# Kernel optimization log

Hardware: AMD Instinct MI355X
Metric: run time of the kernel (lower is better)

## Reference

```python
import jax, jax.numpy as jnp
import numpy as np

N = 30000      # nodes
E = 480000     # edges (avg degree 16)
IN = 128       # input_size
HID = 128      # hidden_size
H = 4          # heads
C = HID // H   # channels per head = 32
NEG_SLOPE = 0.2


def gat_layer(x, src, dst, W, al, ar, act):
    """DGL-style GATConv: x (N, Fin) -> (N, h*c). al, ar: (h, c)."""
    n = x.shape[0]
    h, c = al.shape
    f = (x @ W).reshape(n, h, c)                      # projected features
    el = jnp.sum(f * al, axis=-1)                     # (N, h)
    er = jnp.sum(f * ar, axis=-1)                     # (N, h)
    e = jax.nn.leaky_relu(el[src] + er[dst], NEG_SLOPE)  # (E, h) edge scores
    # edge softmax over incoming edges of each dst node
    m = jax.lax.stop_gradient(jax.ops.segment_max(e, dst, num_segments=n))
    a = jnp.exp(e - m[dst])
    z = jax.ops.segment_sum(a, dst, num_segments=n)   # (N, h)
    alpha = a / z[dst]                                # (E, h)
    out = jax.ops.segment_sum(alpha[:, :, None] * f[src], dst, num_segments=n)
    out = out.reshape(n, h * c)
    return act(out) if act is not None else out


def setup_inputs() -> dict:
    key = jax.random.key(0)
    ks = jax.random.split(key, 14)
    s = 0.1
    return {
        "inputs": jax.random.normal(ks[0], (N, IN), jnp.float32),
        "src": jax.random.randint(ks[1], (E,), 0, N, dtype=jnp.int32),
        "dst": jax.random.randint(ks[2], (E,), 0, N, dtype=jnp.int32),
        "W0": jax.random.normal(ks[3], (IN, H * C), jnp.float32) * s,
        "al0": jax.random.normal(ks[4], (H, C), jnp.float32) * s,
        "ar0": jax.random.normal(ks[5], (H, C), jnp.float32) * s,
        "W1": jax.random.normal(ks[6], (H * C, H * C), jnp.float32) * s,
        "al1": jax.random.normal(ks[7], (H, C), jnp.float32) * s,
        "ar1": jax.random.normal(ks[8], (H, C), jnp.float32) * s,
        "W2": jax.random.normal(ks[9], (H * C, H * HID), jnp.float32) * s,
        "al2": jax.random.normal(ks[10], (H, HID), jnp.float32) * s,
        "ar2": jax.random.normal(ks[11], (H, HID), jnp.float32) * s,
        "fc_w": jax.random.normal(ks[12], (H * HID, 8), jnp.float32) * s,
        "fc_b": jnp.zeros((8,), jnp.float32),
    }


def reference(inputs, src, dst, W0, al0, ar0, W1, al1, ar1, W2, al2, ar2, fc_w, fc_b):
    h = gat_layer(inputs, src, dst, W0, al0, ar0, jax.nn.relu)
    h = gat_layer(h, src, dst, W1, al1, ar1, jax.nn.relu)
    h = gat_layer(h, src, dst, W2, al2, ar2, None)      # (N, H*HID)
    h = jax.nn.relu(h)                                  # dropout p=0 is identity
    pooled = jnp.max(h, axis=0, keepdims=True)          # global max pooling -> (1, H*HID)
    logits = pooled @ fc_w + fc_b                       # (1, 8)
    return jax.nn.softmax(logits, axis=-1)
```

## Files before the change

### kernel.cpp

```cpp
#include <hip/hip_runtime.h>

#define HH 4

typedef __attribute__((ext_vector_type(8))) short bf16x8;
typedef __attribute__((ext_vector_type(4))) float f32x4;

__device__ __forceinline__ float lrelu(float v) { return (v >= 0.0f) ? v : 0.2f * v; }

__device__ __forceinline__ unsigned short f2bf(float x) {
    union { float f; unsigned u; } v; v.f = x;
    unsigned r = (v.u + 0x7FFFu + ((v.u >> 16) & 1u)) >> 16;
    return (unsigned short)r;
}
__device__ __forceinline__ float bf2f(unsigned short b) {
    union { unsigned u; float f; } v; v.u = ((unsigned)b) << 16;
    return v.f;
}

__global__ void zero_kernel(int* __restrict__ p, int n) {
    int i = blockIdx.x * blockDim.x + threadIdx.x;
    if (i < n) p[i] = 0;
}

__global__ void hist_kernel(const int* __restrict__ dst, int* __restrict__ deg, int E) {
    int i = blockIdx.x * blockDim.x + threadIdx.x;
    if (i < E) atomicAdd(&deg[dst[i]], 1);
}

__global__ void scan_block(const int* __restrict__ deg, int* __restrict__ rs,
                           int* __restrict__ bsum, int n) {
    __shared__ int buf[1024];
    int i = blockIdx.x * 1024 + threadIdx.x;
    int v = (i < n) ? deg[i] : 0;
    buf[threadIdx.x] = v;
    __syncthreads();
    for (int off = 1; off < 1024; off <<= 1) {
        int t = (threadIdx.x >= off) ? buf[threadIdx.x - off] : 0;
        __syncthreads();
        buf[threadIdx.x] += t;
        __syncthreads();
    }
    if (i < n) rs[i + 1] = buf[threadIdx.x];
    if (threadIdx.x == 1023) bsum[blockIdx.x] = buf[1023];
}

__global__ void scan_top(int* bsum, int nb) {
    if (threadIdx.x == 0 && blockIdx.x == 0) {
        int acc = 0;
        for (int b = 0; b < nb; ++b) { int t = bsum[b]; bsum[b] = acc; acc += t; }
    }
}

__global__ void scan_add(int* __restrict__ rs, const int* __restrict__ bsum, int n) {
    int i = blockIdx.x * blockDim.x + threadIdx.x;
    if (i == 0) rs[0] = 0;
    if (i < n) rs[i + 1] += bsum[i >> 10];
}

__global__ void scatter_kernel(const int* __restrict__ src, const int* __restrict__ dst,
                               const int* __restrict__ rs, int* __restrict__ cur,
                               int* __restrict__ csrc, int E) {
    int i = blockIdx.x * blockDim.x + threadIdx.x;
    if (i >= E) return;
    int d = dst[i];
    int p = rs[d] + atomicAdd(&cur[d], 1);
    csrc[p] = src[i];
}

__global__ void prep_all(const float* __restrict__ W0, const float* __restrict__ W1,
                         const float* __restrict__ W2, const float* __restrict__ al2,
                         const float* __restrict__ ar2, bf16x8* __restrict__ WFH,
                         bf16x8* __restrict__ WFL, float* __restrict__ wl,
                         float* __restrict__ wr) {
    if (blockIdx.x < 48) {
        const int wid = blockIdx.x * 4 + (threadIdx.x >> 6);
        const int l = threadIdx.x & 63;
        const int lr = l & 15, lg = l >> 4;
        int t = wid;
        const float* srcp;
        int stride, coff;
        if (t < 32) { srcp = W0; stride = 128; coff = 0; }
        else if (t < 64) { srcp = W1; stride = 128; coff = 0; t -= 32; }
        else { t -= 64; srcp = W2; stride = 512; coff = (t >> 5) * 128; t &= 31; }
        const int kt = t >> 3, ct = t & 7;
        bf16x8 h8, l8;
#pragma unroll
        for (int j = 0; j < 8; ++j) {
            float w = srcp[(size_t)(kt * 32 + lg * 8 + j) * stride + coff + ct * 16 + lr];
            unsigned short hb = f2bf(w);
            h8[j] = (short)hb;
            l8[j] = (short)f2bf(w - bf2f(hb));
        }
        WFH[(size_t)wid * 64 + l] = h8;
        WFL[(size_t)wid * 64 + l] = l8;
    } else {
        int idx = threadIdx.x;
#pragma unroll
        for (int k = 0; k < 2; ++k, idx += 256) {
            int h = idx >> 7, i = idx & 127;
            float sl = 0.0f, sr = 0.0f;
            for (int c = 0; c < 128; ++c) {
                float w = W2[(size_t)i * 512 + h * 128 + c];
                sl = fmaf(w, al2[h * 128 + c], sl);
                sr = fmaf(w, ar2[h * 128 + c], sr);
            }
            wl[idx] = sl;
            wr[idx] = sr;
        }
    }
}

__global__ __launch_bounds__(256) void mfma_gemm128(const float* __restrict__ x,
                                                    const bf16x8* __restrict__ BH,
                                                    const bf16x8* __restrict__ BL,
                                                    unsigned short* __restrict__ fbf,
                                                    const float* __restrict__ al,
                                                    const float* __restrict__ ar,
                                                    float* __restrict__ el,
                                                    float* __restrict__ er, int n) {
    const int tid = threadIdx.x;
    const int w = tid >> 6, l = tid & 63;
    const int lr = l & 15, lg = l >> 4;
    const int rowbase = blockIdx.x * 64 + w * 16;
    const int arow = rowbase + lr;

    f32x4 acc[8];
#pragma unroll
    for (int ct = 0; ct < 8; ++ct) acc[ct] = (f32x4){0.f, 0.f, 0.f, 0.f};

    for (int kt = 0; kt < 4; ++kt) {
        float a[8];
        if (arow < n) {
            float4 p0 = *reinterpret_cast<const float4*>(&x[(size_t)arow * 128 + kt * 32 + lg * 8]);
            float4 p1 = *reinterpret_cast<const float4*>(&x[(size_t)arow * 128 + kt * 32 + lg * 8 + 4]);
            a[0] = p0.x; a[1] = p0.y; a[2] = p0.z; a[3] = p0.w;
            a[4] = p1.x; a[5] = p1.y; a[6] = p1.z; a[7] = p1.w;
        } else {
#pragma unroll
            for (int j = 0; j < 8; ++j) a[j] = 0.f;
        }
        bf16x8 ah, alo;
#pragma unroll
        for (int j = 0; j < 8; ++j) {
            unsigned short hb = f2bf(a[j]);
            ah[j] = (short)hb;
            alo[j] = (short)f2bf(a[j] - bf2f(hb));
        }
        const bf16x8* bh = &BH[(size_t)(kt * 8) * 64 + l];
        const bf16x8* bl = &BL[(size_t)(kt * 8) * 64 + l];
#pragma unroll
        for (int ct = 0; ct < 8; ++ct) {
            bf16x8 b1 = bh[ct * 64];
            bf16x8 b2 = bl[ct * 64];
            acc[ct] = __builtin_amdgcn_mfma_f32_16x16x32_bf16(ah, b1, acc[ct], 0, 0, 0);
            acc[ct] = __builtin_amdgcn_mfma_f32_16x16x32_bf16(alo, b1, acc[ct], 0, 0, 0);
            acc[ct] = __builtin_amdgcn_mfma_f32_16x16x32_bf16(ah, b2, acc[ct], 0, 0, 0);
        }
    }
#pragma unroll
    for (int reg = 0; reg < 4; ++reg) {
        int orow = rowbase + lg * 4 + reg;
        if (orow < n) {
#pragma unroll
            for (int ct = 0; ct < 8; ++ct)
                fbf[(size_t)orow * 128 + ct * 16 + lr] = f2bf(acc[ct][reg]);
        }
    }
    float pel[4][4], per_[4][4];
#pragma unroll
    for (int h = 0; h < 4; ++h) {
        float a0 = al[h * 32 + lr], a1 = al[h * 32 + 16 + lr];
        float r0 = ar[h * 32 + lr], r1 = ar[h * 32 + 16 + lr];
#pragma unroll
        for (int reg = 0; reg < 4; ++reg) {
            pel[reg][h] = acc[2 * h][reg] * a0 + acc[2 * h + 1][reg] * a1;
            per_[reg][h] = acc[2 * h][reg] * r0 + acc[2 * h + 1][reg] * r1;
        }
    }
#pragma unroll
    for (int off = 1; off < 16; off <<= 1) {
#pragma unroll
        for (int reg = 0; reg < 4; ++reg)
#pragma unroll
            for (int h = 0; h < 4; ++h) {
                pel[reg][h] += __shfl_xor(pel[reg][h], off);
                per_[reg][h] += __shfl_xor(per_[reg][h], off);
            }
    }
    if (lr == 0) {
#pragma unroll
        for (int reg = 0; reg < 4; ++reg) {
            int orow = rowbase + lg * 4 + reg;
            if (orow < n) {
#pragma unroll
                for (int h = 0; h < 4; ++h) {
                    el[orow * HH + h] = pel[reg][h];
                    er[orow * HH + h] = per_[reg][h];
                }
            }
        }
    }
}

__global__ __launch_bounds__(256) void mfma_bd_pool(const unsigned short* __restrict__ aggbf,
                                                    const bf16x8* __restrict__ WFH,
                                                    const bf16x8* __restrict__ WFL,
                                                    unsigned* __restrict__ pooled, int n) {
    __shared__ float smax[4][128];
    const int tid = threadIdx.x;
    const int w = tid >> 6, l = tid & 63;
    const int lr = l & 15, lg = l >> 4;
    const int y = blockIdx.y;
    const int rowbase = blockIdx.x * 64 + w * 16;
    const int arow = rowbase + lr;
    const bf16x8* BH = WFH + (size_t)(64 + y * 32) * 64;
    const bf16x8* BL = WFL + (size_t)(64 + y * 32) * 64;

    f32x4 acc[8];
#pragma unroll
    for (int ct = 0; ct < 8; ++ct) acc[ct] = (f32x4){0.f, 0.f, 0.f, 0.f};

    for (int kt = 0; kt < 4; ++kt) {
        bf16x8 av = {0, 0, 0, 0, 0, 0, 0, 0};
        if (arow < n)
            av = *reinterpret_cast<const bf16x8*>(&aggbf[(size_t)arow * 512 + y * 128 + kt * 32 + lg * 8]);
        const bf16x8* bh = &BH[(size_t)(kt * 8) * 64 + l];
        const bf16x8* bl = &BL[(size_t)(kt * 8) * 64 + l];
#pragma unroll
        for (int ct = 0; ct < 8; ++ct) {
            acc[ct] = __builtin_amdgcn_mfma_f32_16x16x32_bf16(av, bh[ct * 64], acc[ct], 0, 0, 0);
            acc[ct] = __builtin_amdgcn_mfma_f32_16x16x32_bf16(av, bl[ct * 64], acc[ct], 0, 0, 0);
        }
    }
    float cm[8];
#pragma unroll
    for (int ct = 0; ct < 8; ++ct) {
        float v = fmaxf(fmaxf(acc[ct][0], acc[ct][1]), fmaxf(acc[ct][2], acc[ct][3]));
        cm[ct] = fmaxf(v, 0.f);
    }
#pragma unroll
    for (int ct = 0; ct < 8; ++ct) {
        cm[ct] = fmaxf(cm[ct], __shfl_xor(cm[ct], 16));
        cm[ct] = fmaxf(cm[ct], __shfl_xor(cm[ct], 32));
    }
    if (l < 16) {
#pragma unroll
        for (int ct = 0; ct < 8; ++ct) smax[w][ct * 16 + lr] = cm[ct];
    }
    __syncthreads();
    if (tid < 128) {
        float mx = fmaxf(fmaxf(smax[0][tid], smax[1][tid]), fmaxf(smax[2][tid], smax[3][tid]));
        atomicMax(&pooled[y * 128 + tid], __float_as_uint(mx));
    }
}

template <int MODE>
__global__ __launch_bounds__(256) void aggr_wave128(const int* __restrict__ rs,
                                                    const int* __restrict__ csrc,
                                                    const float* __restrict__ el,
                                                    const float* __restrict__ er,
                                                    const unsigned short* __restrict__ fbf,
                                                    float* __restrict__ out,
                                                    unsigned short* __restrict__ outbf,
                                                    const float* __restrict__ wl,
                                                    const float* __restrict__ wr,
                                                    float* __restrict__ el2,
                                                    float* __restrict__ er2, int n) {
    const int d = blockIdx.x * 4 + (threadIdx.x >> 6);
    if (d >= n) return;
    const int lane = threadIdx.x & 63;
    const int hg = lane >> 4, j16 = lane & 15;
    const int hw = lane >> 5;
    const int L31 = lane & 31;
    const int cb4 = L31 * 4;
    const int myh = L31 >> 3;
    const int e0 = rs[d], e1 = rs[d + 1];
    const float erd = er[d * HH + hg];

    float4 acc = {0.f, 0.f, 0.f, 0.f};
    float zacc = 0.f;
    for (int c0 = e0; c0 < e1; c0 += 16) {
        const int cnt = min(16, e1 - c0);
        int s_mine = 0;
        float wmine = 0.f;
        if (j16 < cnt) {
            s_mine = csrc[c0 + j16];
            wmine = __expf(lrelu(el[s_mine * HH + hg] + erd));
        }
        zacc += wmine;
        const int pairs = cnt >> 1;
#pragma unroll 4
        for (int jj = 0; jj < pairs; ++jj) {
            int idx = 2 * jj + hw;
            int s = __shfl(s_mine, idx);
            float wv = __shfl(wmine, myh * 16 + idx);
            ushort4 xu = *reinterpret_cast<const ushort4*>(&fbf[(size_t)s * 128 + cb4]);
            acc.x = fmaf(wv, bf2f(xu.x), acc.x);
            acc.y = fmaf(wv, bf2f(xu.y), acc.y);
            acc.z = fmaf(wv, bf2f(xu.z), acc.z);
            acc.w = fmaf(wv, bf2f(xu.w), acc.w);
        }
        if (cnt & 1) {
            int idx = cnt - 1;
            int s = __shfl(s_mine, idx);
            float wv = __shfl(wmine, myh * 16 + idx);
            if (hw) wv = 0.f;
            ushort4 xu = *reinterpret_cast<const ushort4*>(&fbf[(size_t)s * 128 + cb4]);
            acc.x = fmaf(wv, bf2f(xu.x), acc.x);
            acc.y = fmaf(wv, bf2f(xu.y), acc.y);
            acc.z = fmaf(wv, bf2f(xu.z), acc.z);
            acc.w = fmaf(wv, bf2f(xu.w), acc.w);
        }
    }
    float zh = zacc;
#pragma unroll
    for (int off = 1; off < 16; off <<= 1) zh += __shfl_xor(zh, off);
    float zmy = __shfl(zh, myh * 16);
    const float rz = (zmy > 0.f) ? 1.0f / zmy : 0.f;
    acc.x += __shfl_xor(acc.x, 32);
    acc.y += __shfl_xor(acc.y, 32);
    acc.z += __shfl_xor(acc.z, 32);
    acc.w += __shfl_xor(acc.w, 32);
    acc.x = fmaxf(acc.x * rz, 0.f);
    acc.y = fmaxf(acc.y * rz, 0.f);
    acc.z = fmaxf(acc.z * rz, 0.f);
    acc.w = fmaxf(acc.w * rz, 0.f);
    if (MODE == 0) {
        if (hw == 0) *reinterpret_cast<float4*>(&out[(size_t)d * 128 + cb4]) = acc;
    } else {
        if (hw == 0) {
            ushort4 sv;
            sv.x = f2bf(acc.x); sv.y = f2bf(acc.y); sv.z = f2bf(acc.z); sv.w = f2bf(acc.w);
            *reinterpret_cast<ushort4*>(&outbf[(size_t)d * 128 + cb4]) = sv;
        }
        float pl[4], pr[4];
#pragma unroll
        for (int h = 0; h < 4; ++h) {
            float4 wlv = *reinterpret_cast<const float4*>(&wl[h * 128 + cb4]);
            float4 wrv = *reinterpret_cast<const float4*>(&wr[h * 128 + cb4]);
            pl[h] = acc.x * wlv.x + acc.y * wlv.y + acc.z * wlv.z + acc.w * wlv.w;
            pr[h] = acc.x * wrv.x + acc.y * wrv.y + acc.z * wrv.z + acc.w * wrv.w;
        }
#pragma unroll
        for (int off = 1; off < 32; off <<= 1) {
#pragma unroll
            for (int h = 0; h < 4; ++h) {
                pl[h] += __shfl_xor(pl[h], off);
                pr[h] += __shfl_xor(pr[h], off);
            }
        }
        if (lane == 0) {
#pragma unroll
            for (int h = 0; h < 4; ++h) {
                el2[d * HH + h] = pl[h];
                er2[d * HH + h] = pr[h];
            }
        }
    }
}

__global__ __launch_bounds__(256) void aggr_x(const int* __restrict__ rs,
                                              const int* __restrict__ csrc,
                                              const float* __restrict__ el,
                                              const float* __restrict__ er,
                                              const unsigned short* __restrict__ xbf,
                                              unsigned short* __restrict__ aggbf, int n) {
    const int d = blockIdx.x * 4 + (threadIdx.x >> 6);
    if (d >= n) return;
    const int lane = threadIdx.x & 63;
    const int hg = lane >> 4, j16 = lane & 15;
    const int hw = lane >> 5;
    const int L31 = lane & 31;
    const int cb4 = L31 * 4;
    const int e0 = rs[d], e1 = rs[d + 1];
    const float erd = er[d * HH + hg];

    float4 acc[4];
#pragma unroll
    for (int h = 0; h < 4; ++h) acc[h] = (float4){0.f, 0.f, 0.f, 0.f};
    float zacc = 0.f;
    for (int c0 = e0; c0 < e1; c0 += 16) {
        const int cnt = min(16, e1 - c0);
        int s_mine = 0;
        float wmine = 0.f;
        if (j16 < cnt) {
            s_mine = csrc[c0 + j16];
            wmine = __expf(lrelu(el[s_mine * HH + hg] + erd));
        }
        zacc += wmine;
        const int pairs = cnt >> 1;
#pragma unroll 2
        for (int jj = 0; jj < pairs; ++jj) {
            int idx = 2 * jj + hw;
            int s = __shfl(s_mine, idx);
            float w0 = __shfl(wmine, idx);
            float w1 = __shfl(wmine, 16 + idx);
            float w2 = __shfl(wmine, 32 + idx);
            float w3 = __shfl(wmine, 48 + idx);
            ushort4 xu = *reinterpret_cast<const ushort4*>(&xbf[(size_t)s * 128 + cb4]);
            float x0 = bf2f(xu.x), x1 = bf2f(xu.y), x2 = bf2f(xu.z), x3 = bf2f(xu.w);
            acc[0].x = fmaf(w0, x0, acc[0].x); acc[0].y = fmaf(w0, x1, acc[0].y);
            acc[0].z = fmaf(w0, x2, acc[0].z); acc[0].w = fmaf(w0, x3, acc[0].w);
            acc[1].x = fmaf(w1, x0, acc[1].x); acc[1].y = fmaf(w1, x1, acc[1].y);
            acc[1].z = fmaf(w1, x2, acc[1].z); acc[1].w = fmaf(w1, x3, acc[1].w);
            acc[2].x = fmaf(w2, x0, acc[2].x); acc[2].y = fmaf(w2, x1, acc[2].y);
            acc[2].z = fmaf(w2, x2, acc[2].z); acc[2].w = fmaf(w2, x3, acc[2].w);
            acc[3].x = fmaf(w3, x0, acc[3].x); acc[3].y = fmaf(w3, x1, acc[3].y);
            acc[3].z = fmaf(w3, x2, acc[3].z); acc[3].w = fmaf(w3, x3, acc[3].w);
        }
        if (cnt & 1) {
            int idx = cnt - 1;
            int s = __shfl(s_mine, idx);
            float m = hw ? 0.f : 1.f;
            float w0 = m * __shfl(wmine, idx);
            float w1 = m * __shfl(wmine, 16 + idx);
            float w2 = m * __shfl(wmine, 32 + idx);
            float w3 = m * __shfl(wmine, 48 + idx);
            ushort4 xu = *reinterpret_cast<const ushort4*>(&xbf[(size_t)s * 128 + cb4]);
            float x0 = bf2f(xu.x), x1 = bf2f(xu.y), x2 = bf2f(xu.z), x3 = bf2f(xu.w);
            acc[0].x = fmaf(w0, x0, acc[0].x); acc[0].y = fmaf(w0, x1, acc[0].y);
            acc[0].z = fmaf(w0, x2, acc[0].z); acc[0].w = fmaf(w0, x3, acc[0].w);
            acc[1].x = fmaf(w1, x0, acc[1].x); acc[1].y = fmaf(w1, x1, acc[1].y);
            acc[1].z = fmaf(w1, x2, acc[1].z); acc[1].w = fmaf(w1, x3, acc[1].w);
            acc[2].x = fmaf(w2, x0, acc[2].x); acc[2].y = fmaf(w2, x1, acc[2].y);
            acc[2].z = fmaf(w2, x2, acc[2].z); acc[2].w = fmaf(w2, x3, acc[2].w);
            acc[3].x = fmaf(w3, x0, acc[3].x); acc[3].y = fmaf(w3, x1, acc[3].y);
            acc[3].z = fmaf(w3, x2, acc[3].z); acc[3].w = fmaf(w3, x3, acc[3].w);
        }
    }
    float zh = zacc;
#pragma unroll
    for (int off = 1; off < 16; off <<= 1) zh += __shfl_xor(zh, off);
    float rzh[4];
#pragma unroll
    for (int h = 0; h < 4; ++h) {
        float zv = __shfl(zh, h * 16);
        rzh[h] = (zv > 0.f) ? 1.0f / zv : 0.f;
    }
#pragma unroll
    for (int h = 0; h < 4; ++h) {
        acc[h].x += __shfl_xor(acc[h].x, 32);
        acc[h].y += __shfl_xor(acc[h].y, 32);
        acc[h].z += __shfl_xor(acc[h].z, 32);
        acc[h].w += __shfl_xor(acc[h].w, 32);
        acc[h].x *= rzh[h]; acc[h].y *= rzh[h]; acc[h].z *= rzh[h]; acc[h].w *= rzh[h];
    }
    if (hw == 0) {
#pragma unroll
        for (int h = 0; h < 4; ++h) {
            ushort4 sv;
            sv.x = f2bf(acc[h].x); sv.y = f2bf(acc[h].y);
            sv.z = f2bf(acc[h].z); sv.w = f2bf(acc[h].w);
            *reinterpret_cast<ushort4*>(&aggbf[(size_t)d * 512 + h * 128 + cb4]) = sv;
        }
    }
}

__global__ void head_kernel(const float* __restrict__ pooled, const float* __restrict__ fcw,
                            const float* __restrict__ fcb, float* __restrict__ out) {
    __shared__ float logits[8];
    int t = threadIdx.x;
    if (t < 8) {
        float acc = fcb[t];
        for (int i = 0; i < 512; ++i) acc = fmaf(pooled[i], fcw[i * 8 + t], acc);
        logits[t] = acc;
    }
    __syncthreads();
    if (t == 0) {
        float mx = -1e30f;
        for (int j = 0; j < 8; ++j) mx = fmaxf(mx, logits[j]);
        float ex[8], s = 0.0f;
        for (int j = 0; j < 8; ++j) { ex[j] = expf(logits[j] - mx); s += ex[j]; }
        for (int j = 0; j < 8; ++j) out[j] = ex[j] / s;
    }
}

extern "C" void kernel_launch(void* const* d_in, const int* in_sizes, int n_in,
                              void* d_out, int out_size, void* d_ws, size_t ws_size,
                              hipStream_t stream) {
    const float* x0  = (const float*)d_in[0];
    const int*   src = (const int*)d_in[1];
    const int*   dst = (const int*)d_in[2];
    const float* W0  = (const float*)d_in[3];
    const float* al0 = (const float*)d_in[4];
    const float* ar0 = (const float*)d_in[5];
    const float* W1  = (const float*)d_in[6];
    const float* al1 = (const float*)d_in[7];
    const float* ar1 = (const float*)d_in[8];
    const float* W2  = (const float*)d_in[9];
    const float* al2 = (const float*)d_in[10];
    const float* ar2 = (const float*)d_in[11];
    const float* fcw = (const float*)d_in[12];
    const float* fcb = (const float*)d_in[13];
    float* outp = (float*)d_out;

    const int N = in_sizes[0] / 128;
    const int E = in_sizes[1];

    float* B0   = (float*)d_ws;
    float* el   = B0 + (size_t)N * 128;
    float* er   = el + (size_t)N * HH;
    float* el2  = er + (size_t)N * HH;
    float* er2  = el2 + (size_t)N * HH;
    float* wl   = er2 + (size_t)N * HH;
    float* wr   = wl + 512;
    int* deg  = (int*)(wr + 512);
    int* cur  = deg + N;
    float* pooled = (float*)(cur + N);
    int* rs   = (int*)(pooled + 512);
    int* bsum = rs + (N + 1);
    int* csrc = bsum + 64;
    unsigned short* Fbf   = (unsigned short*)(csrc + E);
    unsigned short* B1bf  = Fbf + (size_t)N * 128;
    unsigned short* AGGbf = B1bf + (size_t)N * 128;
    uintptr_t wfaddr = ((uintptr_t)(AGGbf + (size_t)N * 512) + 15) & ~(uintptr_t)15;
    bf16x8* WFH = (bf16x8*)wfaddr;
    bf16x8* WFL = WFH + (size_t)192 * 64;

    const int nzero = 2 * N + 512;
    zero_kernel<<<(nzero + 255) / 256, 256, 0, stream>>>(deg, nzero);
    prep_all<<<49, 256, 0, stream>>>(W0, W1, W2, al2, ar2, WFH, WFL, wl, wr);
    hist_kernel<<<(E + 255) / 256, 256, 0, stream>>>(dst, deg, E);
    const int nb = (N + 1023) / 1024;
    scan_block<<<nb, 1024, 0, stream>>>(deg, rs, bsum, N);
    scan_top<<<1, 64, 0, stream>>>(bsum, nb);
    scan_add<<<(N + 255) / 256, 256, 0, stream>>>(rs, bsum, N);
    scatter_kernel<<<(E + 255) / 256, 256, 0, stream>>>(src, dst, rs, cur, csrc, E);

    const int rowTiles = (N + 63) / 64;
    const int nodeBlocks = (N + 3) / 4;

    mfma_gemm128<<<rowTiles, 256, 0, stream>>>(x0, WFH, WFL, Fbf, al0, ar0, el, er, N);
    aggr_wave128<0><<<nodeBlocks, 256, 0, stream>>>(rs, csrc, el, er, Fbf, B0, nullptr,
                                                    nullptr, nullptr, nullptr, nullptr, N);
    mfma_gemm128<<<rowTiles, 256, 0, stream>>>(B0, WFH + (size_t)32 * 64, WFL + (size_t)32 * 64,
                                               Fbf, al1, ar1, el, er, N);
    aggr_wave128<1><<<nodeBlocks, 256, 0, stream>>>(rs, csrc, el, er, Fbf, nullptr, B1bf,
                                                    wl, wr, el2, er2, N);
    aggr_x<<<nodeBlocks, 256, 0, stream>>>(rs, csrc, el2, er2, B1bf, AGGbf, N);
    mfma_bd_pool<<<dim3(rowTiles, 4), 256, 0, stream>>>(AGGbf, WFH, WFL, (unsigned*)pooled, N);

    head_kernel<<<1, 64, 0, stream>>>(pooled, fcw, fcb, outp);
}
```

Before: 263.7 us.

## Process one edge per iteration across full wavefront in GAT aggregation kernels

Both aggregation kernels drop the 16-edge chunked scheme with shuffles and half-wave splitting. Instead every lane walks all incoming edges itself and recomputes the edge weight, and the row range is made wave-uniform with readfirstlane. In aggr_wave128 each lane now owns 2 channels, so no cross-half reduction is needed. In aggr_x each lane handles 8 channels of one head. This removes shuffle and reduction overhead, but every lane now repeats the csrc/el loads and the exp per edge, and the edge-level parallelism that hid gather latency is lost.

```diff
diff --git a/kernel.cpp b/kernel.cpp
--- a/kernel.cpp
+++ b/kernel.cpp
@@ -14,6 +14,14 @@
 }
 __device__ __forceinline__ float bf2f(unsigned short b) {
     union { unsigned u; float f; } v; v.u = ((unsigned)b) << 16;
+    return v.f;
+}
+__device__ __forceinline__ float bf2f_lo(unsigned u) {
+    union { unsigned x; float f; } v; v.x = u << 16;
+    return v.f;
+}
+__device__ __forceinline__ float bf2f_hi(unsigned u) {
+    union { unsigned x; float f; } v; v.x = u & 0xffff0000u;
     return v.f;
 }
 
@@ -266,83 +274,46 @@
                                                     const float* __restrict__ wr,
                                                     float* __restrict__ el2,
                                                     float* __restrict__ er2, int n) {
-    const int d = blockIdx.x * 4 + (threadIdx.x >> 6);
+    int d = blockIdx.x * 4 + (threadIdx.x >> 6);
     if (d >= n) return;
+    d = __builtin_amdgcn_readfirstlane(d);
     const int lane = threadIdx.x & 63;
-    const int hg = lane >> 4, j16 = lane & 15;
-    const int hw = lane >> 5;
-    const int L31 = lane & 31;
-    const int cb4 = L31 * 4;
-    const int myh = L31 >> 3;
-    const int e0 = rs[d], e1 = rs[d + 1];
+    const int hg = lane >> 4;
+    const int cb2 = lane * 2;
+    const int e0 = __builtin_amdgcn_readfirstlane(rs[d]);
+    const int e1 = __builtin_amdgcn_readfirstlane(rs[d + 1]);
     const float erd = er[d * HH + hg];
 
-    float4 acc = {0.f, 0.f, 0.f, 0.f};
-    float zacc = 0.f;
-    for (int c0 = e0; c0 < e1; c0 += 16) {
-        const int cnt = min(16, e1 - c0);
-        int s_mine = 0;
-        float wmine = 0.f;
-        if (j16 < cnt) {
-            s_mine = csrc[c0 + j16];
-            wmine = __expf(lrelu(el[s_mine * HH + hg] + erd));
-        }
-        zacc += wmine;
-        const int pairs = cnt >> 1;
+    float z = 0.f, a0 = 0.f, a1 = 0.f;
 #pragma unroll 4
-        for (int jj = 0; jj < pairs; ++jj) {
-            int idx = 2 * jj + hw;
-            int s = __shfl(s_mine, idx);
-            float wv = __shfl(wmine, myh * 16 + idx);
-            ushort4 xu = *reinterpret_cast<const ushort4*>(&fbf[(size_t)s * 128 + cb4]);
-            acc.x = fmaf(wv, bf2f(xu.x), acc.x);
-            acc.y = fmaf(wv, bf2f(xu.y), acc.y);
-            acc.z = fmaf(wv, bf2f(xu.z), acc.z);
-            acc.w = fmaf(wv, bf2f(xu.w), acc.w);
-        }
-        if (cnt & 1) {
-            int idx = cnt - 1;
-            int s = __shfl(s_mine, idx);
-            float wv = __shfl(wmine, myh * 16 + idx);
-            if (hw) wv = 0.f;
-            ushort4 xu = *reinterpret_cast<const ushort4*>(&fbf[(size_t)s * 128 + cb4]);
-            acc.x = fmaf(wv, bf2f(xu.x), acc.x);
-            acc.y = fmaf(wv, bf2f(xu.y), acc.y);
-            acc.z = fmaf(wv, bf2f(xu.z), acc.z);
-            acc.w = fmaf(wv, bf2f(xu.w), acc.w);
-        }
-    }
-    float zh = zacc;
-#pragma unroll
-    for (int off = 1; off < 16; off <<= 1) zh += __shfl_xor(zh, off);
-    float zmy = __shfl(zh, myh * 16);
-    const float rz = (zmy > 0.f) ? 1.0f / zmy : 0.f;
-    acc.x += __shfl_xor(acc.x, 32);
-    acc.y += __shfl_xor(acc.y, 32);
-    acc.z += __shfl_xor(acc.z, 32);
-    acc.w += __shfl_xor(acc.w, 32);
-    acc.x = fmaxf(acc.x * rz, 0.f);
-    acc.y = fmaxf(acc.y * rz, 0.f);
-    acc.z = fmaxf(acc.z * rz, 0.f);
-    acc.w = fmaxf(acc.w * rz, 0.f);
+    for (int e = e0; e < e1; ++e) {
+        int s = csrc[e];
+        float v = el[s * HH + hg] + erd;
+        float wv = __expf(lrelu(v));
+        z += wv;
+        unsigned xu = *reinterpret_cast<const unsigned*>(&fbf[(size_t)s * 128 + cb2]);
+        a0 = fmaf(wv, bf2f_lo(xu), a0);
+        a1 = fmaf(wv, bf2f_hi(xu), a1);
+    }
+    const float rz = (z > 0.f) ? 1.0f / z : 0.f;
+    a0 = fmaxf(a0 * rz, 0.f);
+    a1 = fmaxf(a1 * rz, 0.f);
     if (MODE == 0) {
-        if (hw == 0) *reinterpret_cast<float4*>(&out[(size_t)d * 128 + cb4]) = acc;
+        *reinterpret_cast<float2*>(&out[(size_t)d * 128 + cb2]) = make_float2(a0, a1);
     } else {
-        if (hw == 0) {
-            ushort4 sv;
-            sv.x = f2bf(acc.x); sv.y = f2bf(acc.y); sv.z = f2bf(acc.z); sv.w = f2bf(acc.w);
-            *reinterpret_cast<ushort4*>(&outbf[(size_t)d * 128 + cb4]) = sv;
-        }
+        ushort2 sv;
+        sv.x = f2bf(a0); sv.y = f2bf(a1);
+        *reinterpret_cast<ushort2*>(&outbf[(size_t)d * 128 + cb2]) = sv;
         float pl[4], pr[4];
 #pragma unroll
         for (int h = 0; h < 4; ++h) {
-            float4 wlv = *reinterpret_cast<const float4*>(&wl[h * 128 + cb4]);
-            float4 wrv = *reinterpret_cast<const float4*>(&wr[h * 128 + cb4]);
-            pl[h] = acc.x * wlv.x + acc.y * wlv.y + acc.z * wlv.z + acc.w * wlv.w;
-            pr[h] = acc.x * wrv.x + acc.y * wrv.y + acc.z * wrv.z + acc.w * wrv.w;
-        }
-#pragma unroll
-        for (int off = 1; off < 32; off <<= 1) {
+            float2 wlv = *reinterpret_cast<const float2*>(&wl[h * 128 + cb2]);
+            float2 wrv = *reinterpret_cast<const float2*>(&wr[h * 128 + cb2]);
+            pl[h] = a0 * wlv.x + a1 * wlv.y;
+            pr[h] = a0 * wrv.x + a1 * wrv.y;
+        }
+#pragma unroll
+        for (int off = 1; off < 64; off <<= 1) {
 #pragma unroll
             for (int h = 0; h < 4; ++h) {
                 pl[h] += __shfl_xor(pl[h], off);
@@ -365,95 +336,44 @@
                                               const float* __restrict__ er,
                                               const unsigned short* __restrict__ xbf,
                                               unsigned short* __restrict__ aggbf, int n) {
-    const int d = blockIdx.x * 4 + (threadIdx.x >> 6);
+    int d = blockIdx.x * 4 + (threadIdx.x >> 6);
     if (d >= n) return;
+    d = __builtin_amdgcn_readfirstlane(d);
     const int lane = threadIdx.x & 63;
     const int hg = lane >> 4, j16 = lane & 15;
-    const int hw = lane >> 5;
-    const int L31 = lane & 31;
-    const int cb4 = L31 * 4;
-    const int e0 = rs[d], e1 = rs[d + 1];
+    const int e0 = __builtin_amdgcn_readfirstlane(rs[d]);
+    const int e1 = __builtin_amdgcn_readfirstlane(rs[d + 1]);
     const float erd = er[d * HH + hg];
 
-    float4 acc[4];
-#pragma unroll
-    for (int h = 0; h < 4; ++h) acc[h] = (float4){0.f, 0.f, 0.f, 0.f};
-    float zacc = 0.f;
-    for (int c0 = e0; c0 < e1; c0 += 16) {
-        const int cnt = min(16, e1 - c0);
-        int s_mine = 0;
-        float wmine = 0.f;
-        if (j16 < cnt) {
-            s_mine = csrc[c0 + j16];
-            wmine = __expf(lrelu(el[s_mine * HH + hg] + erd));
-        }
-        zacc += wmine;
-        const int pairs = cnt >> 1;
+    float z = 0.f;
+    float acc[8];
+#pragma unroll
+    for (int j = 0; j < 8; ++j) acc[j] = 0.f;
 #pragma unroll 2
-        for (int jj = 0; jj < pairs; ++jj) {
-            int idx = 2 * jj + hw;
-            int s = __shfl(s_mine, idx);
-            float w0 = __shfl(wmine, idx);
-            float w1 = __shfl(wmine, 16 + idx);
-            float w2 = __shfl(wmine, 32 + idx);
-            float w3 = __shfl(wmine, 48 + idx);
-            ushort4 xu = *reinterpret_cast<const ushort4*>(&xbf[(size_t)s * 128 + cb4]);
-            float x0 = bf2f(xu.x), x1 = bf2f(xu.y), x2 = bf2f(xu.z), x3 = bf2f(xu.w);
-            acc[0].x = fmaf(w0, x0, acc[0].x); acc[0].y = fmaf(w0, x1, acc[0].y);
-            acc[0].z = fmaf(w0, x2, acc[0].z); acc[0].w = fmaf(w0, x3, acc[0].w);
-            acc[1].x = fmaf(w1, x0, acc[1].x); acc[1].y = fmaf(w1, x1, acc[1].y);
-            acc[1].z = fmaf(w1, x2, acc[1].z); acc[1].w = fmaf(w1, x3, acc[1].w);
-            acc[2].x = fmaf(w2, x0, acc[2].x); acc[2].y = fmaf(w2, x1, acc[2].y);
-            acc[2].z = fmaf(w2, x2, acc[2].z); acc[2].w = fmaf(w2, x3, acc[2].w);
-            acc[3].x = fmaf(w3, x0, acc[3].x); acc[3].y = fmaf(w3, x1, acc[3].y);
-            acc[3].z = fmaf(w3, x2, acc[3].z); acc[3].w = fmaf(w3, x3, acc[3].w);
-        }
-        if (cnt & 1) {
-            int idx = cnt - 1;
-            int s = __shfl(s_mine, idx);
-            float m = hw ? 0.f : 1.f;
-            float w0 = m * __shfl(wmine, idx);
-            float w1 = m * __shfl(wmine, 16 + idx);
-            float w2 = m * __shfl(wmine, 32 + idx);
-            float w3 = m * __shfl(wmine, 48 + idx);
-            ushort4 xu = *reinterpret_cast<const ushort4*>(&xbf[(size_t)s * 128 + cb4]);
-            float x0 = bf2f(xu.x), x1 = bf2f(xu.y), x2 = bf2f(xu.z), x3 = bf2f(xu.w);
-            acc[0].x = fmaf(w0, x0, acc[0].x); acc[0].y = fmaf(w0, x1, acc[0].y);
-            acc[0].z = fmaf(w0, x2, acc[0].z); acc[0].w = fmaf(w0, x3, acc[0].w);
-            acc[1].x = fmaf(w1, x0, acc[1].x); acc[1].y = fmaf(w1, x1, acc[1].y);
-            acc[1].z = fmaf(w1, x2, acc[1].z); acc[1].w = fmaf(w1, x3, acc[1].w);
-            acc[2].x = fmaf(w2, x0, acc[2].x); acc[2].y = fmaf(w2, x1, acc[2].y);
-            acc[2].z = fmaf(w2, x2, acc[2].z); acc[2].w = fmaf(w2, x3, acc[2].w);
-            acc[3].x = fmaf(w3, x0, acc[3].x); acc[3].y = fmaf(w3, x1, acc[3].y);
-            acc[3].z = fmaf(w3, x2, acc[3].z); acc[3].w = fmaf(w3, x3, acc[3].w);
-        }
-    }
-    float zh = zacc;
-#pragma unroll
-    for (int off = 1; off < 16; off <<= 1) zh += __shfl_xor(zh, off);
-    float rzh[4];
-#pragma unroll
-    for (int h = 0; h < 4; ++h) {
-        float zv = __shfl(zh, h * 16);
-        rzh[h] = (zv > 0.f) ? 1.0f / zv : 0.f;
-    }
-#pragma unroll
-    for (int h = 0; h < 4; ++h) {
-        acc[h].x += __shfl_xor(acc[h].x, 32);
-        acc[h].y += __shfl_xor(acc[h].y, 32);
-        acc[h].z += __shfl_xor(acc[h].z, 32);
-        acc[h].w += __shfl_xor(acc[h].w, 32);
-        acc[h].x *= rzh[h]; acc[h].y *= rzh[h]; acc[h].z *= rzh[h]; acc[h].w *= rzh[h];
-    }
-    if (hw == 0) {
-#pragma unroll
-        for (int h = 0; h < 4; ++h) {
-            ushort4 sv;
-            sv.x = f2bf(acc[h].x); sv.y = f2bf(acc[h].y);
-            sv.z = f2bf(acc[h].z); sv.w = f2bf(acc[h].w);
-            *reinterpret_cast<ushort4*>(&aggbf[(size_t)d * 512 + h * 128 + cb4]) = sv;
-        }
-    }
+    for (int e = e0; e < e1; ++e) {
+        int s = csrc[e];
+        float v = el[s * HH + hg] + erd;
+        float wv = __expf(lrelu(v));
+        z += wv;
+        uint4 xu = *reinterpret_cast<const uint4*>(&xbf[(size_t)s * 128 + j16 * 8]);
+        acc[0] = fmaf(wv, bf2f_lo(xu.x), acc[0]);
+        acc[1] = fmaf(wv, bf2f_hi(xu.x), acc[1]);
+        acc[2] = fmaf(wv, bf2f_lo(xu.y), acc[2]);
+        acc[3] = fmaf(wv, bf2f_hi(xu.y), acc[3]);
+        acc[4] = fmaf(wv, bf2f_lo(xu.z), acc[4]);
+        acc[5] = fmaf(wv, bf2f_hi(xu.z), acc[5]);
+        acc[6] = fmaf(wv, bf2f_lo(xu.w), acc[6]);
+        acc[7] = fmaf(wv, bf2f_hi(xu.w), acc[7]);
+    }
+    const float rz = (z > 0.f) ? 1.0f / z : 0.f;
+    ushort4 s0, s1;
+    s0.x = f2bf(acc[0] * rz); s0.y = f2bf(acc[1] * rz);
+    s0.z = f2bf(acc[2] * rz); s0.w = f2bf(acc[3] * rz);
+    s1.x = f2bf(acc[4] * rz); s1.y = f2bf(acc[5] * rz);
+    s1.z = f2bf(acc[6] * rz); s1.w = f2bf(acc[7] * rz);
+    unsigned short* op = &aggbf[(size_t)d * 512 + hg * 128 + j16 * 8];
+    *reinterpret_cast<ushort4*>(op) = s0;
+    *reinterpret_cast<ushort4*>(op + 4) = s1;
 }
 
 __global__ void head_kernel(const float* __restrict__ pooled, const float* __restrict__ fcw,
```

New measurement: 244.0 us. 7.4% less time.
